# Performance work log

Hardware: AMD Instinct MI355X
Metric: run time of the kernel (lower is better)

The kernel has to match this reference:

```python
import jax, jax.numpy as jnp
import numpy as np

N = 12288   # nodes
E = 393216  # edges (avg degree 32)
B = 16      # graphs in batch
F_IN = 15   # node feature dim
H = 32      # hidden_dim
EMB = 64    # embedding_dim
NC = 11     # num_classes
EDIM = 2    # edge feature dim
EPS = 1e-5  # BatchNorm eps


def _bn(x, gamma, beta):
    # training-mode BatchNorm1d: biased batch variance, matches torch normalization
    mu = jnp.mean(x, axis=0)
    var = jnp.var(x, axis=0)
    return gamma * (x - mu) * jax.lax.rsqrt(var + EPS) + beta


def setup_inputs() -> dict:
    key = jax.random.key(0)
    ks = jax.random.split(key, 16)
    def p(k, shape, s=0.05):
        return jax.random.normal(k, shape, dtype=jnp.float32) * s
    z = lambda *s: jnp.zeros(s, jnp.float32)
    o = lambda *s: jnp.ones(s, jnp.float32)
    return {
        "x": jax.random.normal(ks[0], (N, F_IN), dtype=jnp.float32),
        "edge_attr": jax.random.normal(ks[1], (E, EDIM), dtype=jnp.float32),
        "w_edge": p(ks[2], (EDIM, 1)), "b_edge": z(1),
        "w1": p(ks[3], (F_IN, H)), "b1": z(H), "g1": o(H), "be1": z(H),
        "w2": p(ks[4], (H, 2 * H)), "b2": z(2 * H), "g2": o(2 * H), "be2": z(2 * H),
        "w3": p(ks[5], (2 * H, EMB)), "b3": z(EMB), "g3": o(EMB), "be3": z(EMB),
        "wf1": p(ks[6], (EMB, 512)), "bf1": z(512), "gf1": o(512), "bef1": z(512),
        "wf2": p(ks[7], (512, 256)), "bf2": z(256), "gf2": o(256), "bef2": z(256),
        "wf3": p(ks[8], (256, NC)), "bf3": z(NC),
        "edge_index": jax.random.randint(ks[9], (2, E), 0, N, dtype=jnp.int64)
                      if jax.config.jax_enable_x64 else jax.random.randint(ks[9], (2, E), 0, N),
        "batch": jnp.sort(jax.random.randint(ks[10], (N,), 0, B)),
    }


def reference(x, edge_attr, w_edge, b_edge,
              w1, b1, g1, be1, w2, b2, g2, be2, w3, b3, g3, be3,
              wf1, bf1, gf1, bef1, wf2, bf2, gf2, bef2, wf3, bf3,
              edge_index, batch):
    # edge weights: sigmoid(Linear(edge_attr)) -> [E]
    ew = jax.nn.sigmoid(edge_attr @ w_edge + b_edge)[:, 0]
    # dense adjacency with self loops, accumulate duplicates (sparse_coo.to_dense)
    loop = jnp.arange(N)
    row = jnp.concatenate([edge_index[0], loop])
    col = jnp.concatenate([edge_index[1], loop])
    w_aug = jnp.concatenate([ew, jnp.ones((N,), ew.dtype)])
    adj = jnp.zeros((N, N), ew.dtype).at[row, col].add(w_aug)
    # symmetric degree normalization D^-1/2 A D^-1/2
    deg = adj.sum(axis=1)
    dis = jnp.where(deg > 0, jax.lax.rsqrt(jnp.where(deg > 0, deg, 1.0)), 0.0)
    support = dis[:, None] * adj * dis[None, :]
    # three GCN layers: support @ x @ W + b, BN, relu
    h = jax.nn.relu(_bn(support @ x @ w1 + b1, g1, be1))
    h = jax.nn.relu(_bn(support @ h @ w2 + b2, g2, be2))
    h = jax.nn.relu(_bn(support @ h @ w3 + b3, g3, be3))
    # global max pool per graph (empty graphs -> zeros)
    seg = jax.ops.segment_max(h, batch, num_segments=B)
    cnt = jax.ops.segment_sum(jnp.ones((N,), h.dtype), batch, num_segments=B)
    emb = jnp.where(cnt[:, None] > 0, seg, 0.0)
    # MLP head (dropout = identity at inference)
    o = jax.nn.relu(_bn(emb @ wf1 + bf1, gf1, bef1))
    o = jax.nn.relu(_bn(o @ wf2 + bf2, gf2, bef2))
    logits = o @ wf3 + bf3
    return jax.nn.log_softmax(logits, axis=1), emb
```

## Files before the change

kernel.cpp:

```cpp
#include <hip/hip_runtime.h>
#include <hip/hip_bf16.h>

#define NN   12288
#define EE   393216
#define WELL 128
#define NELL (NN*WELL)
#define BG   16
#define FIN  15
#define FH1  32
#define FH2  64
#define NCL  11
#define BNEPS 1e-5f
#define NBANK 32

typedef unsigned long long u64;
static inline int cdiv(long a, long b){ return (int)((a + b - 1) / b); }

__device__ __forceinline__ int getIdx(const void* p, long i, int is64){
  return is64 ? (int)((const long long*)p)[i] : ((const int*)p)[i];
}

__device__ __forceinline__ float degOf(unsigned lo){
  return 1.0f + (float)lo * (1.0f/1048576.0f);
}

__global__ void k_pre(u64* deg_cnt, float* csp1, float* csp2, float* csp3,
                      float* embf, const void* ei, const void* batch, int* flags){
  int g = blockIdx.x*256 + threadIdx.x;
  if (g < NN) deg_cnt[g] = 0ull;
  if (g < NBANK*128){ csp1[g] = 0.f; csp2[g] = 0.f; csp3[g] = 0.f; }
  if (g < BG*64) embf[g] = 0.f;
  if (blockIdx.x == 0 && threadIdx.x < 64){
    const int* a = (const int*)ei;
    unsigned long long m0 = __ballot(a[2*threadIdx.x + 1] == 0);
    const int* b = (const int*)batch;
    int j = 96*threadIdx.x;
    unsigned long long m1 = __ballot(b[2*j + 1] == 0);
    if (threadIdx.x == 0){
      flags[0] = (m0 == ~0ull) ? 1 : 0;
      flags[1] = (m1 == ~0ull) ? 1 : 0;
    }
  }
}

__global__ void k_edge(const float* ea, const float* we, const float* bedg,
                       const void* ei, const int* flags, u64* deg_cnt,
                       unsigned* csr_p){
  int e = blockIdx.x*256 + threadIdx.x;
  if (e >= EE) return;
  int is64 = flags[0];
  float2 eav = ((const float2*)ea)[e];
  float z = eav.x*we[0] + eav.y*we[1] + bedg[0];
  float w = 1.0f/(1.0f + expf(-z));
  int r = getIdx(ei, e, is64);
  int c = getIdx(ei, (long)EE + e, is64);
  u64 add = (1ull << 32) | (u64)__float2uint_rn(w * 1048576.0f);
  u64 old = atomicAdd(&deg_cnt[r], add);
  int slot = (int)(old >> 32);
  if (slot < WELL){
    unsigned wfix = __float2uint_rn(w * 131072.0f);
    csr_p[((long)r << 7) + slot] = (unsigned)c | (wfix << 14);
  }
}

__global__ void __launch_bounds__(256) k_fix2(const u64* __restrict__ deg_cnt,
                                              unsigned* __restrict__ csr_p){
  int row = blockIdx.x*4 + (threadIdx.x >> 6);
  int lane = threadIdx.x & 63;
  const unsigned* cl = (const unsigned*)deg_cnt;
  int n = (int)(deg_cnt[row] >> 32);
  n = n < WELL ? n : WELL;
  for (int s = lane; s < n; s += 64){
    long idx = ((long)row << 7) + s;
    unsigned v = csr_p[idx];
    int c = (int)(v & 16383u);
    float w = (float)(v >> 14) * (1.0f/131072.0f);
    w *= rsqrtf(degOf(cl[2*c]));
    csr_p[idx] = (unsigned)c | (__float2uint_rn(w * 131072.0f) << 14);
  }
}

template<int F, int FP, int FO, int APPLY_BN>
__global__ void __launch_bounds__(256) k_layer(
    const float* __restrict__ Hin,
    const float* __restrict__ cspin, const float* __restrict__ gam,
    const float* __restrict__ bet,
    const float* __restrict__ W, const float* __restrict__ bias,
    const u64* __restrict__ deg_cnt, const unsigned* __restrict__ csr_p,
    float* __restrict__ Pout, float* __restrict__ csout){
  const int R = 256/FP;
  __shared__ float At[R][FP];
  __shared__ float lcs[FO], lcq[FO];
  __shared__ float lsc[64], lsh[64];
  if (threadIdx.x < FO){ lcs[threadIdx.x] = 0.f; lcq[threadIdx.x] = 0.f; }
  if (APPLY_BN && threadIdx.x < F){
    float s = 0.f, q = 0.f;
    #pragma unroll
    for (int b = 0; b < NBANK; b++){
      s += cspin[b*128 + threadIdx.x];
      q += cspin[b*128 + 64 + threadIdx.x];
    }
    float mu  = s*(1.0f/NN);
    float var = q*(1.0f/NN) - mu*mu;
    float sc = gam[threadIdx.x]*rsqrtf(var + BNEPS);
    lsc[threadIdx.x] = sc;
    lsh[threadIdx.x] = bet[threadIdx.x] - mu*sc;
  }
  __syncthreads();
  int f = threadIdx.x % FP, lr = threadIdx.x / FP;
  float sc = 1.f, sh = 0.f;
  if (APPLY_BN && f < F){ sc = lsc[f]; sh = lsh[f]; }
  int row = blockIdx.x*R + lr;
  if (f < F){
    u64 dc = deg_cnt[row];
    float d = rsqrtf(degOf((unsigned)(dc & 0xffffffffull)));
    int n = (int)(dc >> 32);
    n = n < WELL ? n : WELL;
    float v0 = Hin[row*F + f];
    if (APPLY_BN) v0 = fmaxf(v0*sc + sh, 0.f);
    float acc = d * v0;
    int nch = (n + 15) >> 4;
    const uint4* pb = (const uint4*)(csr_p + ((long)row << 7));
    if (nch > 0){
      uint4 a[4], b[4];
      #pragma unroll
      for (int j = 0; j < 4; j++) a[j] = pb[j];
      for (int ch = 0; ch < nch; ch++){
        bool more = (ch + 1 < nch);
        if (more){
          #pragma unroll
          for (int j = 0; j < 4; j++) b[j] = pb[4*ch + 4 + j];
        }
        unsigned pv[16];
        pv[0]=a[0].x; pv[1]=a[0].y; pv[2]=a[0].z; pv[3]=a[0].w;
        pv[4]=a[1].x; pv[5]=a[1].y; pv[6]=a[1].z; pv[7]=a[1].w;
        pv[8]=a[2].x; pv[9]=a[2].y; pv[10]=a[2].z; pv[11]=a[2].w;
        pv[12]=a[3].x; pv[13]=a[3].y; pv[14]=a[3].z; pv[15]=a[3].w;
        int base = ch*16;
        if (base + 16 > n){
          #pragma unroll
          for (int j = 0; j < 16; j++) if (base + j >= n) pv[j] = 0u;
        }
        float hh[16];
        #pragma unroll
        for (int j = 0; j < 16; j++)
          hh[j] = Hin[(int)(pv[j] & 16383u)*F + f];
        #pragma unroll
        for (int j = 0; j < 16; j++){
          float h = hh[j];
          if (APPLY_BN) h = fmaxf(h*sc + sh, 0.f);
          acc += (float)(pv[j] >> 14) * (1.0f/131072.0f) * h;
        }
        if (more){
          #pragma unroll
          for (int j = 0; j < 4; j++) a[j] = b[j];
        }
      }
    }
    At[lr][f] = d * acc;
  }
  __syncthreads();
  const int fo = threadIdx.x % FO;
  float bb = bias[fo];
  for (int o = threadIdx.x; o < R*FO; o += 256){
    int l = o / FO;
    float s = bb;
    #pragma unroll
    for (int fi = 0; fi < F; fi++) s += At[l][fi] * W[fi*FO + fo];
    Pout[(blockIdx.x*R + l)*FO + fo] = s;
    atomicAdd(&lcs[fo], s);
    atomicAdd(&lcq[fo], s*s);
  }
  __syncthreads();
  if (threadIdx.x < FO){
    int bank = blockIdx.x & (NBANK-1);
    atomicAdd(&csout[bank*128 + threadIdx.x],      lcs[threadIdx.x]);
    atomicAdd(&csout[bank*128 + 64 + threadIdx.x], lcq[threadIdx.x]);
  }
}

__global__ void k_pool(const float* P3, const float* csp, const float* gam,
                       const float* bet, const void* batch, const int* flags,
                       float* embf){
  __shared__ float lsc[64], lsh[64];
  if (threadIdx.x < 64){
    float s = 0.f, q = 0.f;
    #pragma unroll
    for (int b = 0; b < NBANK; b++){
      s += csp[b*128 + threadIdx.x];
      q += csp[b*128 + 64 + threadIdx.x];
    }
    float mu  = s*(1.0f/NN);
    float var = q*(1.0f/NN) - mu*mu;
    float sc = gam[threadIdx.x]*rsqrtf(var + BNEPS);
    lsc[threadIdx.x] = sc;
    lsh[threadIdx.x] = bet[threadIdx.x] - mu*sc;
  }
  __syncthreads();
  int is64 = flags[1];
  int b = blockIdx.x & 15, chunk = blockIdx.x >> 4;
  int lo = 0, hi = NN;
  while (lo < hi){ int m = (lo+hi)>>1; if (getIdx(batch, m, is64) < b) lo = m+1; else hi = m; }
  int start = lo;
  lo = start; hi = NN;
  while (lo < hi){ int m = (lo+hi)>>1; if (getIdx(batch, m, is64) < b+1) lo = m+1; else hi = m; }
  int end = lo;
  int f = threadIdx.x & 63, grp = threadIdx.x >> 6;
  float sc = lsc[f], sh = lsh[f];
  float m = 0.0f;
  for (int i = start + chunk*4 + grp; i < end; i += 64)
    m = fmaxf(m, P3[(long)i*FH2 + f]*sc + sh);
  __shared__ float shm[4][64];
  shm[grp][f] = m;
  __syncthreads();
  if (grp == 0){
    float v = fmaxf(fmaxf(shm[0][f], shm[1][f]), fmaxf(shm[2][f], shm[3][f]));
    atomicMax((int*)&embf[b*64 + f], __float_as_int(v));
  }
}

__global__ void __launch_bounds__(256) k_fcA(const float* embf, const float* wf1,
    const float* bf1, const float* gf1, const float* bef1, float* s1g, float* out){
  if (blockIdx.x == 0){
    #pragma unroll
    for (int i = 0; i < 4; i++)
      out[BG*NCL + i*256 + threadIdx.x] = embf[i*256 + threadIdx.x];
  }
  int c = blockIdx.x*4 + (threadIdx.x >> 6);
  int l = threadIdx.x & 63;
  float wcol = wf1[l*512 + c];
  float z[BG];
  #pragma unroll
  for (int r = 0; r < BG; r++){
    float v = embf[r*64 + l] * wcol;
    #pragma unroll
    for (int off = 32; off > 0; off >>= 1) v += __shfl_down(v, off);
    z[r] = v;
  }
  if (l == 0){
    float bb = bf1[c];
    float s = 0.f, q = 0.f;
    #pragma unroll
    for (int r = 0; r < BG; r++){ float zr = z[r] + bb; s += zr; q += zr*zr; }
    float mean = s*(1.f/BG), var = q*(1.f/BG) - mean*mean;
    float inv = rsqrtf(var + BNEPS);
    float gg = gf1[c], b2 = bef1[c];
    #pragma unroll
    for (int r = 0; r < BG; r++)
      s1g[r*512 + c] = fmaxf(gg*(z[r] + bb - mean)*inv + b2, 0.f);
  }
}

__global__ void __launch_bounds__(256) k_fcB(const float* s1g, const float* wf2,
    const float* bf2, const float* gf2, const float* bef2, float* s2g){
  int c = blockIdx.x*4 + (threadIdx.x >> 6);
  int l = threadIdx.x & 63;
  float wreg[8];
  #pragma unroll
  for (int j = 0; j < 8; j++) wreg[j] = wf2[(l + 64*j)*256 + c];
  float z[BG];
  #pragma unroll
  for (int r = 0; r < BG; r++){
    float v = 0.f;
    #pragma unroll
    for (int j = 0; j < 8; j++) v += s1g[r*512 + l + 64*j] * wreg[j];
    #pragma unroll
    for (int off = 32; off > 0; off >>= 1) v += __shfl_down(v, off);
    z[r] = v;
  }
  if (l == 0){
    float bb = bf2[c];
    float s = 0.f, q = 0.f;
    #pragma unroll
    for (int r = 0; r < BG; r++){ float zr = z[r] + bb; s += zr; q += zr*zr; }
    float mean = s*(1.f/BG), var = q*(1.f/BG) - mean*mean;
    float inv = rsqrtf(var + BNEPS);
    float gg = gf2[c], b2 = bef2[c];
    #pragma unroll
    for (int r = 0; r < BG; r++)
      s2g[r*256 + c] = fmaxf(gg*(z[r] + bb - mean)*inv + b2, 0.f);
  }
}

__global__ void k_fc3(const float* s2g, const float* wf3, const float* bf3, float* out){
  __shared__ float s2[BG*256];
  __shared__ float sl[BG*NCL];
  int t = threadIdx.x;
  for (int i = t; i < BG*256; i += 256) s2[i] = s2g[i];
  __syncthreads();
  if (t < BG*NCL){
    int r = t / NCL, c = t - r*NCL;
    float s = bf3[c];
    for (int k = 0; k < 256; k++) s += s2[r*256 + k]*wf3[k*NCL + c];
    sl[t] = s;
  }
  __syncthreads();
  if (t < BG){
    float m = -1e30f;
    for (int c = 0; c < NCL; c++) m = fmaxf(m, sl[t*NCL + c]);
    float s = 0.f;
    for (int c = 0; c < NCL; c++) s += expf(sl[t*NCL + c] - m);
    float lg = logf(s) + m;
    for (int c = 0; c < NCL; c++) out[t*NCL + c] = sl[t*NCL + c] - lg;
  }
}

extern "C" void kernel_launch(void* const* d_in, const int* in_sizes, int n_in,
                              void* d_out, int out_size, void* d_ws, size_t ws_size,
                              hipStream_t stream){
  const float* x    = (const float*)d_in[0];
  const float* ea   = (const float*)d_in[1];
  const float* we   = (const float*)d_in[2];
  const float* bedg = (const float*)d_in[3];
  const float* w1   = (const float*)d_in[4];  const float* b1  = (const float*)d_in[5];
  const float* g1   = (const float*)d_in[6];  const float* be1 = (const float*)d_in[7];
  const float* w2   = (const float*)d_in[8];  const float* b2  = (const float*)d_in[9];
  const float* g2   = (const float*)d_in[10]; const float* be2 = (const float*)d_in[11];
  const float* w3   = (const float*)d_in[12]; const float* b3  = (const float*)d_in[13];
  const float* g3   = (const float*)d_in[14]; const float* be3 = (const float*)d_in[15];
  const float* wf1  = (const float*)d_in[16]; const float* bf1 = (const float*)d_in[17];
  const float* gf1  = (const float*)d_in[18]; const float* bef1= (const float*)d_in[19];
  const float* wf2  = (const float*)d_in[20]; const float* bf2 = (const float*)d_in[21];
  const float* gf2  = (const float*)d_in[22]; const float* bef2= (const float*)d_in[23];
  const float* wf3  = (const float*)d_in[24]; const float* bf3 = (const float*)d_in[25];
  const void* ei    = d_in[26];
  const void* batch = d_in[27];
  float* out = (float*)d_out;

  u64* wq = (u64*)d_ws;
  u64* deg_cnt = wq; wq += NN;
  unsigned* csr_p = (unsigned*)wq; wq += NELL/2;
  float* ws = (float*)wq;
  float* P1    = ws; ws += NN*FH1;
  float* P2    = ws; ws += NN*FH2;
  float* P3    = ws; ws += NN*FH2;
  float* csp1  = ws; ws += NBANK*128;
  float* csp2  = ws; ws += NBANK*128;
  float* csp3  = ws; ws += NBANK*128;
  float* embf  = ws; ws += BG*64;
  float* s1g   = ws; ws += BG*512;
  float* s2g   = ws; ws += BG*256;
  int* flags   = (int*)ws;

  k_pre<<<48, 256, 0, stream>>>(deg_cnt, csp1, csp2, csp3, embf, ei, batch, flags);
  k_edge<<<cdiv(EE,256), 256, 0, stream>>>(ea, we, bedg, ei, flags, deg_cnt, csr_p);
  k_fix2<<<NN/4, 256, 0, stream>>>(deg_cnt, csr_p);

  k_layer<FIN,16,FH1,0><<<NN/16, 256, 0, stream>>>(x, nullptr, nullptr, nullptr,
      w1, b1, deg_cnt, csr_p, P1, csp1);
  k_layer<FH1,32,FH2,1><<<NN/8, 256, 0, stream>>>(P1, csp1, g1, be1,
      w2, b2, deg_cnt, csr_p, P2, csp2);
  k_layer<FH2,64,FH2,1><<<NN/4, 256, 0, stream>>>(P2, csp2, g2, be2,
      w3, b3, deg_cnt, csr_p, P3, csp3);

  k_pool<<<256, 256, 0, stream>>>(P3, csp3, g3, be3, batch, flags, embf);
  k_fcA<<<128, 256, 0, stream>>>(embf, wf1, bf1, gf1, bef1, s1g, out);
  k_fcB<<<64, 256, 0, stream>>>(s1g, wf2, bf2, gf2, bef2, s2g);
  k_fc3<<<1, 256, 0, stream>>>(s2g, wf3, bf3, out);
}
```

Baseline: 228.7 us.

## Split neighbor gather across two lanes per row and apply BN in separate pass

Each row's neighbor aggregation is now shared by two thread groups that take alternating 16-edge chunks, and their partial sums are combined through shared memory. This doubles the grid size per layer and shortens each thread's dependent gather chain. BatchNorm+ReLU is no longer applied on every gathered neighbor value; a separate elementwise kernel normalizes each layer output in place once. The change adds three kernel launches, an extra read and write of each activation buffer, and removes the register prefetch double-buffering of CSR chunks.

```diff
diff --git a/kernel.cpp b/kernel.cpp
--- a/kernel.cpp
+++ b/kernel.cpp
@@ -1,5 +1,4 @@
 #include <hip/hip_runtime.h>
-#include <hip/hip_bf16.h>
 
 #define NN   12288
 #define EE   393216
@@ -80,110 +79,83 @@
   }
 }
 
-template<int F, int FP, int FO, int APPLY_BN>
+template<int F, int FP, int FO>
 __global__ void __launch_bounds__(256) k_layer(
     const float* __restrict__ Hin,
-    const float* __restrict__ cspin, const float* __restrict__ gam,
-    const float* __restrict__ bet,
     const float* __restrict__ W, const float* __restrict__ bias,
     const u64* __restrict__ deg_cnt, const unsigned* __restrict__ csr_p,
     float* __restrict__ Pout, float* __restrict__ csout){
-  const int R = 256/FP;
-  __shared__ float At[R][FP];
+  const int R2 = 256/(FP*2);
+  __shared__ float At[R2][FP];
+  __shared__ float Apart[256];
   __shared__ float lcs[FO], lcq[FO];
-  __shared__ float lsc[64], lsh[64];
-  if (threadIdx.x < FO){ lcs[threadIdx.x] = 0.f; lcq[threadIdx.x] = 0.f; }
-  if (APPLY_BN && threadIdx.x < F){
-    float s = 0.f, q = 0.f;
-    #pragma unroll
-    for (int b = 0; b < NBANK; b++){
-      s += cspin[b*128 + threadIdx.x];
-      q += cspin[b*128 + 64 + threadIdx.x];
-    }
-    float mu  = s*(1.0f/NN);
-    float var = q*(1.0f/NN) - mu*mu;
-    float sc = gam[threadIdx.x]*rsqrtf(var + BNEPS);
-    lsc[threadIdx.x] = sc;
-    lsh[threadIdx.x] = bet[threadIdx.x] - mu*sc;
-  }
-  __syncthreads();
-  int f = threadIdx.x % FP, lr = threadIdx.x / FP;
-  float sc = 1.f, sh = 0.f;
-  if (APPLY_BN && f < F){ sc = lsc[f]; sh = lsh[f]; }
-  int row = blockIdx.x*R + lr;
+  int tid = threadIdx.x;
+  if (tid < FO){ lcs[tid] = 0.f; lcq[tid] = 0.f; }
+  int f = tid % FP;
+  int sub = tid / FP;
+  int kw = sub & 1, lr = sub >> 1;
+  int row = blockIdx.x*R2 + lr;
+  u64 dc = deg_cnt[row];
+  float d = rsqrtf(degOf((unsigned)(dc & 0xffffffffull)));
+  int n = (int)(dc >> 32);
+  n = n < WELL ? n : WELL;
+  float acc = 0.f;
   if (f < F){
-    u64 dc = deg_cnt[row];
-    float d = rsqrtf(degOf((unsigned)(dc & 0xffffffffull)));
-    int n = (int)(dc >> 32);
-    n = n < WELL ? n : WELL;
-    float v0 = Hin[row*F + f];
-    if (APPLY_BN) v0 = fmaxf(v0*sc + sh, 0.f);
-    float acc = d * v0;
+    if (kw == 0) acc = d * Hin[row*F + f];
     int nch = (n + 15) >> 4;
     const uint4* pb = (const uint4*)(csr_p + ((long)row << 7));
-    if (nch > 0){
-      uint4 a[4], b[4];
+    for (int ch = kw; ch < nch; ch += 2){
+      const uint4* pc = pb + 4*ch;
+      uint4 a0 = pc[0], a1 = pc[1], a2 = pc[2], a3 = pc[3];
+      unsigned pv[16];
+      pv[0]=a0.x; pv[1]=a0.y; pv[2]=a0.z; pv[3]=a0.w;
+      pv[4]=a1.x; pv[5]=a1.y; pv[6]=a1.z; pv[7]=a1.w;
+      pv[8]=a2.x; pv[9]=a2.y; pv[10]=a2.z; pv[11]=a2.w;
+      pv[12]=a3.x; pv[13]=a3.y; pv[14]=a3.z; pv[15]=a3.w;
+      int base = ch*16;
+      if (base + 16 > n){
+        #pragma unroll
+        for (int j = 0; j < 16; j++) if (base + j >= n) pv[j] = 0u;
+      }
+      float hh[16];
       #pragma unroll
-      for (int j = 0; j < 4; j++) a[j] = pb[j];
-      for (int ch = 0; ch < nch; ch++){
-        bool more = (ch + 1 < nch);
-        if (more){
-          #pragma unroll
-          for (int j = 0; j < 4; j++) b[j] = pb[4*ch + 4 + j];
-        }
-        unsigned pv[16];
-        pv[0]=a[0].x; pv[1]=a[0].y; pv[2]=a[0].z; pv[3]=a[0].w;
-        pv[4]=a[1].x; pv[5]=a[1].y; pv[6]=a[1].z; pv[7]=a[1].w;
-        pv[8]=a[2].x; pv[9]=a[2].y; pv[10]=a[2].z; pv[11]=a[2].w;
-        pv[12]=a[3].x; pv[13]=a[3].y; pv[14]=a[3].z; pv[15]=a[3].w;
-        int base = ch*16;
-        if (base + 16 > n){
-          #pragma unroll
-          for (int j = 0; j < 16; j++) if (base + j >= n) pv[j] = 0u;
-        }
-        float hh[16];
-        #pragma unroll
-        for (int j = 0; j < 16; j++)
-          hh[j] = Hin[(int)(pv[j] & 16383u)*F + f];
-        #pragma unroll
-        for (int j = 0; j < 16; j++){
-          float h = hh[j];
-          if (APPLY_BN) h = fmaxf(h*sc + sh, 0.f);
-          acc += (float)(pv[j] >> 14) * (1.0f/131072.0f) * h;
-        }
-        if (more){
-          #pragma unroll
-          for (int j = 0; j < 4; j++) a[j] = b[j];
-        }
-      }
+      for (int j = 0; j < 16; j++)
+        hh[j] = Hin[(int)(pv[j] & 16383u)*F + f];
+      #pragma unroll
+      for (int j = 0; j < 16; j++)
+        acc += (float)(pv[j] >> 14) * (1.0f/131072.0f) * hh[j];
     }
-    At[lr][f] = d * acc;
-  }
-  __syncthreads();
-  const int fo = threadIdx.x % FO;
+  }
+  Apart[tid] = acc;
+  __syncthreads();
+  if (f < F && kw == 0)
+    At[lr][f] = d * (Apart[tid] + Apart[tid + FP]);
+  __syncthreads();
+  const int fo = tid % FO;
   float bb = bias[fo];
-  for (int o = threadIdx.x; o < R*FO; o += 256){
+  for (int o = tid; o < R2*FO; o += 256){
     int l = o / FO;
     float s = bb;
     #pragma unroll
     for (int fi = 0; fi < F; fi++) s += At[l][fi] * W[fi*FO + fo];
-    Pout[(blockIdx.x*R + l)*FO + fo] = s;
+    Pout[(blockIdx.x*R2 + l)*FO + fo] = s;
     atomicAdd(&lcs[fo], s);
     atomicAdd(&lcq[fo], s*s);
   }
   __syncthreads();
-  if (threadIdx.x < FO){
+  if (tid < FO){
     int bank = blockIdx.x & (NBANK-1);
-    atomicAdd(&csout[bank*128 + threadIdx.x],      lcs[threadIdx.x]);
-    atomicAdd(&csout[bank*128 + 64 + threadIdx.x], lcq[threadIdx.x]);
-  }
-}
-
-__global__ void k_pool(const float* P3, const float* csp, const float* gam,
-                       const float* bet, const void* batch, const int* flags,
-                       float* embf){
+    atomicAdd(&csout[bank*128 + tid],      lcs[tid]);
+    atomicAdd(&csout[bank*128 + 64 + tid], lcq[tid]);
+  }
+}
+
+template<int F>
+__global__ void __launch_bounds__(256) k_bn(float* __restrict__ P,
+    const float* __restrict__ csp, const float* __restrict__ gam,
+    const float* __restrict__ bet){
   __shared__ float lsc[64], lsh[64];
-  if (threadIdx.x < 64){
+  if (threadIdx.x < F){
     float s = 0.f, q = 0.f;
     #pragma unroll
     for (int b = 0; b < NBANK; b++){
@@ -197,6 +169,19 @@
     lsh[threadIdx.x] = bet[threadIdx.x] - mu*sc;
   }
   __syncthreads();
+  long i4 = (long)blockIdx.x*256 + threadIdx.x;
+  float4* P4 = (float4*)P;
+  float4 v = P4[i4];
+  int c0 = (int)((i4*4) & (F-1));
+  v.x = fmaxf(v.x*lsc[c0]     + lsh[c0],     0.f);
+  v.y = fmaxf(v.y*lsc[c0 + 1] + lsh[c0 + 1], 0.f);
+  v.z = fmaxf(v.z*lsc[c0 + 2] + lsh[c0 + 2], 0.f);
+  v.w = fmaxf(v.w*lsc[c0 + 3] + lsh[c0 + 3], 0.f);
+  P4[i4] = v;
+}
+
+__global__ void k_pool(const float* P3, const void* batch, const int* flags,
+                       float* embf){
   int is64 = flags[1];
   int b = blockIdx.x & 15, chunk = blockIdx.x >> 4;
   int lo = 0, hi = NN;
@@ -206,10 +191,9 @@
   while (lo < hi){ int m = (lo+hi)>>1; if (getIdx(batch, m, is64) < b+1) lo = m+1; else hi = m; }
   int end = lo;
   int f = threadIdx.x & 63, grp = threadIdx.x >> 6;
-  float sc = lsc[f], sh = lsh[f];
   float m = 0.0f;
   for (int i = start + chunk*4 + grp; i < end; i += 64)
-    m = fmaxf(m, P3[(long)i*FH2 + f]*sc + sh);
+    m = fmaxf(m, P3[(long)i*FH2 + f]);
   __shared__ float shm[4][64];
   shm[grp][f] = m;
   __syncthreads();
@@ -346,14 +330,17 @@
   k_edge<<<cdiv(EE,256), 256, 0, stream>>>(ea, we, bedg, ei, flags, deg_cnt, csr_p);
   k_fix2<<<NN/4, 256, 0, stream>>>(deg_cnt, csr_p);
 
-  k_layer<FIN,16,FH1,0><<<NN/16, 256, 0, stream>>>(x, nullptr, nullptr, nullptr,
+  k_layer<FIN,16,FH1><<<NN/8, 256, 0, stream>>>(x,
       w1, b1, deg_cnt, csr_p, P1, csp1);
-  k_layer<FH1,32,FH2,1><<<NN/8, 256, 0, stream>>>(P1, csp1, g1, be1,
+  k_bn<FH1><<<NN*FH1/1024, 256, 0, stream>>>(P1, csp1, g1, be1);
+  k_layer<FH1,32,FH2><<<NN/4, 256, 0, stream>>>(P1,
       w2, b2, deg_cnt, csr_p, P2, csp2);
-  k_layer<FH2,64,FH2,1><<<NN/4, 256, 0, stream>>>(P2, csp2, g2, be2,
+  k_bn<FH2><<<NN*FH2/1024, 256, 0, stream>>>(P2, csp2, g2, be2);
+  k_layer<FH2,64,FH2><<<NN/2, 256, 0, stream>>>(P2,
       w3, b3, deg_cnt, csr_p, P3, csp3);
-
-  k_pool<<<256, 256, 0, stream>>>(P3, csp3, g3, be3, batch, flags, embf);
+  k_bn<FH2><<<NN*FH2/1024, 256, 0, stream>>>(P3, csp3, g3, be3);
+
+  k_pool<<<256, 256, 0, stream>>>(P3, batch, flags, embf);
   k_fcA<<<128, 256, 0, stream>>>(embf, wf1, bf1, gf1, bef1, s1g, out);
   k_fcB<<<64, 256, 0, stream>>>(s1g, wf2, bf2, gf2, bef2, s2g);
   k_fc3<<<1, 256, 0, stream>>>(s2g, wf3, bf3, out);
```

Result: no change. 230.5 us (+0.8%).
